# Kernel tuning notes

Hardware: AMD Instinct MI355X
Metric: run time of the kernel (lower is better)

Reference implementation:

```python
import jax, jax.numpy as jnp
from jax import lax
import numpy as np
import math

B, C, Hf, Wf = 16, 512, 32, 32   # batch, channels, feature map HxW (1024/32)
A, K = 9, 2                      # anchors per location, num classes
NCLU, UNITS, EMB = 100, 512, 128 # cosine-softmax dims
IMG = 1024                       # image side


def setup_inputs() -> dict:
    key = jax.random.key(0)
    ks = jax.random.split(key, 12)
    inp = {}
    inp["features"] = jax.random.normal(ks[0], (B, C, Hf, Wf), jnp.float32)
    inp["anchors"] = jax.random.uniform(ks[1], (Hf * Wf * A, 4), jnp.float32) * IMG
    inp["image_shape"] = IMG
    for l in range(4):
        inp[f"conv_w{l}"] = 0.01 * jax.random.normal(jax.random.fold_in(ks[2], l), (C, C, 3, 3), jnp.float32)
        inp[f"conv_b{l}"] = jnp.zeros((C,), jnp.float32)
    inp["cls_w"] = 0.01 * jax.random.normal(ks[3], (A * K, C, 3, 3), jnp.float32)
    inp["cls_b"] = jnp.full((A * K,), -math.log((1.0 - 0.01) / 0.01), jnp.float32)
    inp["bn_gamma"] = jnp.ones((C,), jnp.float32)
    inp["bn_beta"] = jnp.zeros((C,), jnp.float32)
    inp["proj_w1"] = 0.02 * jax.random.normal(ks[4], (UNITS, C), jnp.float32)
    inp["proj_w2"] = 0.02 * jax.random.normal(ks[5], (UNITS, UNITS), jnp.float32)
    inp["proj_w3"] = 0.02 * jax.random.normal(ks[6], (EMB, UNITS), jnp.float32)
    inp["clusters_w"] = 0.02 * jax.random.normal(ks[7], (NCLU, EMB), jnp.float32)
    inp["fc_scale_w"] = 0.02 * jax.random.normal(ks[8], (1, C), jnp.float32)
    inp["fc_scale_b"] = jnp.zeros((1,), jnp.float32)
    inp["bns_gamma"] = jnp.ones((1,), jnp.float32)
    inp["bns_beta"] = jnp.zeros((1,), jnp.float32)
    return inp


def _conv(x, w, b):
    y = lax.conv_general_dilated(x, w, (1, 1), 'SAME', dimension_numbers=('NCHW', 'OIHW', 'NCHW'))
    return y + b[None, :, None, None]


def _bn(x, g, b, eps=1e-5):  # BatchNorm1d in training mode: batch statistics
    m = x.mean(axis=0)
    v = x.var(axis=0)
    return g * (x - m) * lax.rsqrt(v + eps) + b


def _l2norm(x, axis):  # F.normalize(eps=1e-12)
    n = jnp.linalg.norm(x, axis=axis, keepdims=True)
    return x / jnp.maximum(n, 1e-12)


def reference(features, anchors, conv_w0, conv_b0, conv_w1, conv_b1, conv_w2, conv_b2,
              conv_w3, conv_b3, cls_w, cls_b, bn_gamma, bn_beta, proj_w1, proj_w2,
              proj_w3, clusters_w, fc_scale_w, fc_scale_b, bns_gamma, bns_beta,
              image_shape):
    # --- BBoxClassificationHead ---
    x = features
    for w, b in ((conv_w0, conv_b0), (conv_w1, conv_b1), (conv_w2, conv_b2), (conv_w3, conv_b3)):
        x = jax.nn.relu(_conv(x, w, b))
    logits = _conv(x, cls_w, cls_b)                      # [B, A*K, Hf, Wf]
    N = logits.shape[0]
    logits = logits.reshape(N, A, K, Hf, Wf).transpose(0, 3, 4, 1, 2).reshape(N, Hf * Wf * A, K)

    # --- _get_most_likely_feats: decode anchor centers, argmax foreground prob, gather ---
    feat_size = features.shape[2]
    decim = image_shape // feat_size
    cx = (anchors[:, 2] - anchors[:, 0]) / decim
    cy = (anchors[:, 3] - anchors[:, 1]) / decim
    p_fg = jax.nn.softmax(logits, axis=-1)[..., -1]      # [B, HWA]
    idx = jnp.argmax(p_fg, axis=-1)                      # [B]
    ii = jnp.clip(jnp.round(cy[idx]), 0, feat_size - 1).astype(jnp.int32)
    jj = jnp.clip(jnp.round(cx[idx]), 0, feat_size - 1).astype(jnp.int32)
    local = features[jnp.arange(N), :, ii, jj]           # [B, C]

    # --- CosineModule ---
    h = _bn(local, bn_gamma, bn_beta)
    h = jax.nn.relu(h @ proj_w1.T)
    h = jax.nn.relu(h @ proj_w2.T)
    emb = h @ proj_w3.T
    xn = _l2norm(emb, 1)                                 # [B, EMB]
    wn = _l2norm(clusters_w, 1).T                        # [EMB, NCLU]
    scale = jnp.exp(_bn(local @ fc_scale_w.T + fc_scale_b, bns_gamma, bns_beta))  # [B, 1]
    cosine = scale * (xn @ wn)                           # [B, NCLU]
    return (logits, cosine, xn)
```

## Files before the change

### kernel.cpp

```cpp
#include <hip/hip_runtime.h>

typedef short bf16x8 __attribute__((ext_vector_type(8)));
typedef float f32x4 __attribute__((ext_vector_type(4)));
typedef unsigned int u32x4 __attribute__((ext_vector_type(4)));
typedef unsigned short u16;

__device__ __forceinline__ bool dt_isbf(const void* flagp) {
  return (*(const unsigned int*)flagp) != 0x3F800000u;
}
__device__ __forceinline__ float bf2f(u16 v) {
  unsigned int x = ((unsigned int)v) << 16;
  return __builtin_bit_cast(float, x);
}
__device__ __forceinline__ u16 f2bf(float f) {
  unsigned int x = __builtin_bit_cast(unsigned int, f);
  x += 0x7FFFu + ((x >> 16) & 1u);
  return (u16)(x >> 16);
}
__device__ __forceinline__ float ldf(const void* p, int i, bool bf) {
  return bf ? bf2f(((const u16*)p)[i]) : ((const float*)p)[i];
}
__device__ __forceinline__ void gld_lds16(const void* g, void* l) {
  __builtin_amdgcn_global_load_lds(
      (const __attribute__((address_space(1))) unsigned*)g,
      (__attribute__((address_space(3))) unsigned*)l, 16, 0, 0);
}

__global__ __launch_bounds__(256) void k_to_nhwc(const void* __restrict__ feat,
                                                 u16* __restrict__ outH,
                                                 u16* __restrict__ outL,
                                                 const void* __restrict__ flagp) {
  const bool isbf = dt_isbf(flagp);
  __shared__ float tile[32][33];
  const int b = blockIdx.z, c0 = blockIdx.y << 5, p0 = blockIdx.x << 5;
  const int tp = threadIdx.x & 31, tc = threadIdx.x >> 5;
#pragma unroll
  for (int q = 0; q < 4; ++q) {
    int c = c0 + tc + (q << 3);
    tile[tc + (q << 3)][tp] = ldf(feat, ((b << 9) + c) * 1024 + p0 + tp, isbf);
  }
  __syncthreads();
#pragma unroll
  for (int q = 0; q < 4; ++q) {
    int p = p0 + tc + (q << 3);
    float v = tile[tp][tc + (q << 3)];
    u16 h = f2bf(v);
    int idx = (((b << 10) + p) << 9) + c0 + tp;
    outH[idx] = h;
    if (outL) outL[idx] = f2bf(v - bf2f(h));
  }
}

__global__ __launch_bounds__(256) void k_wtrans(const void* __restrict__ Wsrc,
                                                u16* __restrict__ WTh,
                                                u16* __restrict__ WTl, int Nout,
                                                const void* __restrict__ flagp) {
  const bool isbf = dt_isbf(flagp);
  const int n = blockIdx.x, tid = threadIdx.x;
  __shared__ float Wrow[4608];
  if (n < Nout)
    for (int k = tid; k < 4608; k += 256)
      Wrow[k] = ldf(Wsrc, n * 4608 + k, isbf);
  __syncthreads();
  for (int ko = tid; ko < 4608; ko += 256) {
    float w = 0.f;
    if (n < Nout) {
      int t = ko >> 6, q = (ko >> 3) & 7, j = ko & 7;
      int sk = (t << 6) + ((q ^ (n & 7)) << 3) + j;
      int c = sk & 511, tap = sk >> 9;
      w = Wrow[c * 9 + tap];
    }
    u16 h = f2bf(w);
    WTh[n * 4608 + ko] = h;
    if (!isbf) WTl[n * 4608 + ko] = f2bf(w - bf2f(h));
  }
}

__global__ __launch_bounds__(256) void k_gemm_conv(
    const u16* __restrict__ Xh, const u16* __restrict__ Xl,
    const u16* __restrict__ WTh, const u16* __restrict__ WTl,
    const void* __restrict__ bias,
    u16* __restrict__ Yh, u16* __restrict__ Yl,
    const void* __restrict__ flagp) {
  const bool isbf = dt_isbf(flagp);
  const bool useBL = !isbf;
  const int tid = threadIdx.x;
  const int m0 = blockIdx.x << 7, n0 = blockIdx.y << 7;
  const int b = m0 >> 10, y0 = (m0 & 1023) >> 5;
  __shared__ __align__(16) u16 Ash[13056], Asl[13056];
  __shared__ __align__(16) u16 Bh[8192];
  const int lane = tid & 63, wv = tid >> 6;
  const int wm = wv >> 1, wn = wv & 1;
  const int r16 = lane & 15, lg = lane >> 4;

  f32x4 acc[4][4];
#pragma unroll
  for (int i = 0; i < 4; ++i)
#pragma unroll
    for (int f = 0; f < 4; ++f) acc[i][f] = (f32x4){0.f, 0.f, 0.f, 0.f};

  for (int cb = 0; cb < 8; ++cb) {
    for (int e = tid; e < 1632; e += 256) {
      int pos = e >> 3, c8 = e & 7;
      int yy = pos / 34, xx = pos - yy * 34;
      int y = y0 + yy - 1, x = xx - 1;
      u32x4 vh = {0u, 0u, 0u, 0u}, vl = {0u, 0u, 0u, 0u};
      if ((unsigned)y < 32u && (unsigned)x < 32u) {
        size_t off = (size_t)((((b << 5) + y) << 5) + x) * 512 + (cb << 6) + (c8 << 3);
        vh = *(const u32x4*)(Xh + off);
        vl = *(const u32x4*)(Xl + off);
      }
      int sl = c8 ^ (xx & 7);
      *(u32x4*)(&Ash[(pos << 6) + (sl << 3)]) = vh;
      *(u32x4*)(&Asl[(pos << 6) + (sl << 3)]) = vl;
    }
    for (int tap = 0; tap < 9; ++tap) {
      const int t = (tap << 3) + cb;
#pragma unroll
      for (int issue = 0; issue < 4; ++issue) {
        int cid = (issue << 8) + tid;
        int row = cid >> 3, q = cid & 7;
        gld_lds16(WTh + (size_t)(n0 + row) * 4608 + (t << 6) + (q << 3),
                  &Bh[((issue << 2) + wv) << 9]);
      }
      __syncthreads();
      const int dy = tap / 3 - 1, dx = tap % 3 - 1;
#pragma unroll
      for (int s = 0; s < 2; ++s) {
        bf16x8 ah[4], al[4], bh[4], bl[4];
#pragma unroll
        for (int i = 0; i < 4; ++i) {
          int ar = (wm << 6) + (i << 4) + r16;
          int yy = (ar >> 5) + dy + 1, xx = (ar & 31) + dx + 1;
          int sidx = (s << 2) + lg;
          int ao = ((yy * 34 + xx) << 6) + ((sidx ^ (xx & 7)) << 3);
          ah[i] = *(const bf16x8*)(&Ash[ao]);
          al[i] = *(const bf16x8*)(&Asl[ao]);
          int br = (wn << 6) + (i << 4) + r16;
          int bs_ = sidx ^ (br & 7);
          bh[i] = *(const bf16x8*)(&Bh[(br << 6) + (bs_ << 3)]);
          if (useBL)
            bl[i] = *(const bf16x8*)(WTl + (size_t)(n0 + br) * 4608 + (t << 6) +
                                     (bs_ << 3));
        }
#pragma unroll
        for (int i = 0; i < 4; ++i)
#pragma unroll
          for (int f = 0; f < 4; ++f) {
            acc[i][f] = __builtin_amdgcn_mfma_f32_16x16x32_bf16(ah[i], bh[f], acc[i][f], 0, 0, 0);
            acc[i][f] = __builtin_amdgcn_mfma_f32_16x16x32_bf16(al[i], bh[f], acc[i][f], 0, 0, 0);
            if (useBL)
              acc[i][f] = __builtin_amdgcn_mfma_f32_16x16x32_bf16(ah[i], bl[f], acc[i][f], 0, 0, 0);
          }
      }
      __syncthreads();
    }
  }

#pragma unroll
  for (int f = 0; f < 4; ++f) {
    int col = n0 + (wn << 6) + (f << 4) + r16;
    float bb = ldf(bias, col, isbf);
#pragma unroll
    for (int i = 0; i < 4; ++i) {
      int mb = m0 + (wm << 6) + (i << 4) + (lg << 2);
#pragma unroll
      for (int r = 0; r < 4; ++r) {
        float v = fmaxf(acc[i][f][r] + bb, 0.f);
        size_t o = (size_t)(mb + r) * 512 + col;
        u16 h = f2bf(v);
        Yh[o] = h;
        Yl[o] = f2bf(v - bf2f(h));
      }
    }
  }
}

template <int NB, int KS>
__global__ __launch_bounds__(256) void k_gemm_fast(
    const u16* __restrict__ Xh, const u16* __restrict__ Xl,
    const u16* __restrict__ WTh, const u16* __restrict__ WTl,
    const void* __restrict__ bias, int bias_n,
    u16* __restrict__ Yh, u16* __restrict__ Yl, int Nst, int relu,
    float* __restrict__ Yf, const void* __restrict__ flagp) {
  const bool isbf = dt_isbf(flagp);
  const bool useBL = !isbf;
  const int tid = threadIdx.x;
  const int m0 = blockIdx.x << 7;
  int n0, kt0, kt1;
  if (KS) {
    n0 = 0;
    kt0 = blockIdx.y * 18;
    kt1 = kt0 + 18;
    Yf += (size_t)blockIdx.y * 294912;
  } else {
    n0 = blockIdx.y << 7;
    kt0 = 0;
    kt1 = 72;
  }
  __shared__ __align__(16) u16 Ah[8192], Al[8192], Bh[8192];
  const int lane = tid & 63, wv = tid >> 6;
  const int wm = wv >> 1, wn = wv & 1;
  const int r16 = lane & 15, lg = lane >> 4;

  const int arow0 = tid >> 3, acol = tid & 7;
  int gb[4], gy[4], gx[4];
#pragma unroll
  for (int i = 0; i < 4; ++i) {
    int m = m0 + arow0 + (i << 5);
    gb[i] = m >> 10;
    int p = m & 1023;
    gy[i] = p >> 5;
    gx[i] = p & 31;
  }

  f32x4 acc[4][4];
#pragma unroll
  for (int i = 0; i < 4; ++i)
#pragma unroll
    for (int f = 0; f < 4; ++f) acc[i][f] = (f32x4){0.f, 0.f, 0.f, 0.f};

  for (int t = kt0; t < kt1; ++t) {
    const int tap = t >> 3;
    const int cb = (t & 7) << 6;
    const int dy = tap / 3 - 1, dx = tap % 3 - 1;
    __syncthreads();
#pragma unroll
    for (int issue = 0; issue < NB / 2; ++issue) {
      int cid = (issue << 8) + tid;
      int row = cid >> 3, q = cid & 7;
      const u16* g = WTh + (size_t)(n0 + row) * 4608 + (t << 6) + (q << 3);
      u16* l = &Bh[(size_t)(((issue << 2) + wv) << 6) << 3];
      gld_lds16(g, l);
    }
#pragma unroll
    for (int i = 0; i < 4; ++i) {
      int row = arow0 + (i << 5);
      int ys = gy[i] + dy, xs = gx[i] + dx;
      u32x4 vh = {0u, 0u, 0u, 0u}, vl = {0u, 0u, 0u, 0u};
      if ((unsigned)ys < 32u && (unsigned)xs < 32u) {
        size_t off = (size_t)((((gb[i] << 5) + ys) << 5) + xs) * 512 + cb + (acol << 3);
        vh = *(const u32x4*)(Xh + off);
        vl = *(const u32x4*)(Xl + off);
      }
      int slot = acol ^ (row & 7);
      *(u32x4*)(&Ah[(row << 6) + (slot << 3)]) = vh;
      *(u32x4*)(&Al[(row << 6) + (slot << 3)]) = vl;
    }
    __syncthreads();
#pragma unroll
    for (int s = 0; s < 2; ++s) {
      bf16x8 ah[4], al[4], bh[4], bl[4];
#pragma unroll
      for (int i = 0; i < 4; ++i) {
        int ar = (wm << 6) + (i << 4) + r16;
        int as_ = ((s << 2) + lg) ^ (ar & 7);
        ah[i] = *(const bf16x8*)(&Ah[(ar << 6) + (as_ << 3)]);
        al[i] = *(const bf16x8*)(&Al[(ar << 6) + (as_ << 3)]);
      }
#pragma unroll
      for (int f = 0; f < 4; ++f) {
        if ((wn << 2) + f < NB) {
          int br = (wn << 6) + (f << 4) + r16;
          int bs_ = ((s << 2) + lg) ^ (br & 7);
          bh[f] = *(const bf16x8*)(&Bh[(br << 6) + (bs_ << 3)]);
          if (useBL)
            bl[f] = *(const bf16x8*)(WTl + (size_t)(n0 + br) * 4608 + (t << 6) +
                                     ((((s << 2) + lg) ^ (br & 7)) << 3));
        }
      }
#pragma unroll
      for (int i = 0; i < 4; ++i)
#pragma unroll
        for (int f = 0; f < 4; ++f) {
          if ((wn << 2) + f < NB) {
            acc[i][f] = __builtin_amdgcn_mfma_f32_16x16x32_bf16(ah[i], bh[f], acc[i][f], 0, 0, 0);
            acc[i][f] = __builtin_amdgcn_mfma_f32_16x16x32_bf16(al[i], bh[f], acc[i][f], 0, 0, 0);
            if (useBL)
              acc[i][f] = __builtin_amdgcn_mfma_f32_16x16x32_bf16(ah[i], bl[f], acc[i][f], 0, 0, 0);
          }
        }
    }
  }

#pragma unroll
  for (int f = 0; f < 4; ++f) {
    if ((wn << 2) + f >= NB) continue;
    int col = n0 + (wn << 6) + (f << 4) + r16;
    if (col < Nst) {
      float bb = (col < bias_n) ? ldf(bias, col, isbf) : 0.f;
#pragma unroll
      for (int i = 0; i < 4; ++i) {
        int mb = m0 + (wm << 6) + (i << 4) + (lg << 2);
#pragma unroll
        for (int r = 0; r < 4; ++r) {
          float v = acc[i][f][r] + bb;
          if (relu) v = fmaxf(v, 0.f);
          size_t o = (size_t)(mb + r) * Nst + col;
          if (Yh) {
            u16 h = f2bf(v);
            Yh[o] = h;
            Yl[o] = f2bf(v - bf2f(h));
          }
          if (Yf) Yf[o] = v;
        }
      }
    }
  }
}

__global__ __launch_bounds__(256) void k_cls_fin(const float* __restrict__ PART,
                                                 const void* __restrict__ bias,
                                                 float* __restrict__ out,
                                                 const void* __restrict__ flagp) {
  const bool isbf = dt_isbf(flagp);
  int o = blockIdx.x * 256 + threadIdx.x;
  if (o < 294912) {
    float v = PART[o] + PART[294912 + o] + PART[2 * 294912 + o] +
              PART[3 * 294912 + o];
    out[o] = v + ldf(bias, o % 18, isbf);
  }
}

__global__ __launch_bounds__(256) void k_gemm_slow(
    const u16* __restrict__ Xh, const u16* __restrict__ Xl,
    const void* __restrict__ Wsrc, const void* __restrict__ bias, int bias_n,
    u16* __restrict__ Yh, u16* __restrict__ Yl, int Nst, int relu,
    float* __restrict__ Yf, const void* __restrict__ flagp) {
  const bool isbf = dt_isbf(flagp);
  const bool hasBL = !isbf;
  const bool hasAL = (Xl != nullptr);
  const int tid = threadIdx.x;
  const int m0 = blockIdx.x << 7, n0 = blockIdx.y << 7;
  __shared__ __align__(16) u16 Ah[128 * 72];
  __shared__ __align__(16) u16 Al[128 * 72];
  __shared__ __align__(16) u16 Bh[128 * 72];
  __shared__ __align__(16) u16 Bl[128 * 72];
  const int lane = tid & 63, wvi = tid >> 6;
  const int wm = wvi >> 1, wn = wvi & 1;
  const int r16 = lane & 15, lg = lane >> 4;
  f32x4 acc[4][4];
#pragma unroll
  for (int i = 0; i < 4; ++i)
#pragma unroll
    for (int f = 0; f < 4; ++f) acc[i][f] = (f32x4){0.f, 0.f, 0.f, 0.f};
  for (int t = 0; t < 72; ++t) {
    const int tap = t >> 3, cb = (t & 7) << 6;
    const int dy = tap / 3 - 1, dx = tap % 3 - 1;
    __syncthreads();
    for (int e = tid; e < 4096; e += 256) {
      int row = e >> 5, kc2 = e & 31;
      int m = m0 + row;
      int b = m >> 10, p = m & 1023;
      int ys = (p >> 5) + dy, xs = (p & 31) + dx;
      unsigned vh = 0u, vl = 0u;
      if ((unsigned)ys < 32u && (unsigned)xs < 32u) {
        int off = ((((b << 5) + ys) << 5) + xs) * 512 + cb + (kc2 << 1);
        vh = *(const unsigned*)(Xh + off);
        if (hasAL) vl = *(const unsigned*)(Xl + off);
      }
      *(unsigned*)(&Ah[row * 72 + (kc2 << 1)]) = vh;
      if (hasAL) *(unsigned*)(&Al[row * 72 + (kc2 << 1)]) = vl;
    }
    for (int e = tid; e < 4096; e += 256) {
      int row = e >> 5, kc2 = e & 31;
      int n = n0 + row;
      unsigned ph = 0u, pl = 0u;
      if (n < bias_n) {
        int c = cb + (kc2 << 1);
        float w0 = ldf(Wsrc, ((n << 9) + c) * 9 + tap, isbf);
        float w1 = ldf(Wsrc, ((n << 9) + c + 1) * 9 + tap, isbf);
        u16 h0 = f2bf(w0), h1 = f2bf(w1);
        ph = ((unsigned)h1 << 16) | (unsigned)h0;
        if (hasBL) {
          u16 l0 = f2bf(w0 - bf2f(h0)), l1 = f2bf(w1 - bf2f(h1));
          pl = ((unsigned)l1 << 16) | (unsigned)l0;
        }
      }
      *(unsigned*)(&Bh[row * 72 + (kc2 << 1)]) = ph;
      if (hasBL) *(unsigned*)(&Bl[row * 72 + (kc2 << 1)]) = pl;
    }
    __syncthreads();
#pragma unroll
    for (int s = 0; s < 2; ++s) {
      bf16x8 ah[4], al[4], bh[4], bl[4];
#pragma unroll
      for (int i = 0; i < 4; ++i) {
        int ao = ((wm << 6) + (i << 4) + r16) * 72 + (s << 5) + (lg << 3);
        int bo = ((wn << 6) + (i << 4) + r16) * 72 + (s << 5) + (lg << 3);
        ah[i] = *(const bf16x8*)(&Ah[ao]);
        bh[i] = *(const bf16x8*)(&Bh[bo]);
        if (hasAL) al[i] = *(const bf16x8*)(&Al[ao]);
        if (hasBL) bl[i] = *(const bf16x8*)(&Bl[bo]);
      }
#pragma unroll
      for (int i = 0; i < 4; ++i)
#pragma unroll
        for (int f = 0; f < 4; ++f) {
          acc[i][f] = __builtin_amdgcn_mfma_f32_16x16x32_bf16(ah[i], bh[f], acc[i][f], 0, 0, 0);
          if (hasAL)
            acc[i][f] = __builtin_amdgcn_mfma_f32_16x16x32_bf16(al[i], bh[f], acc[i][f], 0, 0, 0);
          if (hasBL)
            acc[i][f] = __builtin_amdgcn_mfma_f32_16x16x32_bf16(ah[i], bl[f], acc[i][f], 0, 0, 0);
        }
    }
  }
#pragma unroll
  for (int f = 0; f < 4; ++f) {
    int col = n0 + (wn << 6) + (f << 4) + r16;
    if (col < Nst) {
      float bb = (col < bias_n) ? ldf(bias, col, isbf) : 0.f;
#pragma unroll
      for (int i = 0; i < 4; ++i) {
        int mb = m0 + (wm << 6) + (i << 4) + (lg << 2);
#pragma unroll
        for (int r = 0; r < 4; ++r) {
          float v = acc[i][f][r] + bb;
          if (relu) v = fmaxf(v, 0.f);
          int o = (mb + r) * Nst + col;
          if (Yh) {
            u16 h = f2bf(v);
            Yh[o] = h;
            if (Yl) Yl[o] = f2bf(v - bf2f(h));
          }
          if (Yf) Yf[o] = v;
        }
      }
    }
  }
}

__global__ __launch_bounds__(256) void k_pick(const float* __restrict__ LG,
                                              const void* __restrict__ anchors,
                                              const int* __restrict__ imgshape,
                                              const void* __restrict__ feat,
                                              float* __restrict__ local,
                                              const void* __restrict__ flagp) {
  const bool isbf = dt_isbf(flagp);
  const int n = blockIdx.x, tid = threadIdx.x;
  float bs = -1e30f;
  int bj = 0x7FFFFFFF;
  for (int j = tid; j < 9216; j += 256) {
    float s = LG[n * 18432 + j * 2 + 1] - LG[n * 18432 + j * 2];
    if (s > bs) { bs = s; bj = j; }
  }
  __shared__ float ss[256];
  __shared__ int sj[256];
  ss[tid] = bs; sj[tid] = bj;
  __syncthreads();
  for (int off = 128; off; off >>= 1) {
    if (tid < off) {
      if (ss[tid + off] > ss[tid] ||
          (ss[tid + off] == ss[tid] && sj[tid + off] < sj[tid])) {
        ss[tid] = ss[tid + off]; sj[tid] = sj[tid + off];
      }
    }
    __syncthreads();
  }
  __shared__ int sij[2];
  if (tid == 0) {
    int idx = sj[0];
    float a0 = ldf(anchors, idx * 4 + 0, isbf);
    float a1 = ldf(anchors, idx * 4 + 1, isbf);
    float a2 = ldf(anchors, idx * 4 + 2, isbf);
    float a3 = ldf(anchors, idx * 4 + 3, isbf);
    int iv = imgshape[0];
    float fimg = (iv > 0 && iv < (1 << 24)) ? (float)iv
                                            : __builtin_bit_cast(float, iv);
    float decim = floorf(fimg / 32.f);
    float cx = (a2 - a0) / decim, cy = (a3 - a1) / decim;
    int ii = (int)fminf(fmaxf(rintf(cy), 0.f), 31.f);
    int jj = (int)fminf(fmaxf(rintf(cx), 0.f), 31.f);
    sij[0] = ii; sij[1] = jj;
  }
  __syncthreads();
  const int ii = sij[0], jj = sij[1];
  for (int c = tid; c < 512; c += 256)
    local[(n << 9) + c] = ldf(feat, ((n << 9) + c) * 1024 + (ii << 5) + jj, isbf);
}

__global__ __launch_bounds__(256) void k_head_pre(
    const float* __restrict__ local, const void* bn_g, const void* bn_b,
    const void* fcw, const void* fcb, const void* bsg, const void* bsb,
    const void* clus, float* __restrict__ HS, float* __restrict__ SCAL,
    float* __restrict__ CN, const void* __restrict__ flagp) {
  const bool isbf = dt_isbf(flagp);
  const int tid = threadIdx.x, blk = blockIdx.x;
  if (blk < 2) {
    int c = (blk << 8) + tid;
    float xv[16];
    float m = 0.f;
#pragma unroll
    for (int n = 0; n < 16; ++n) { xv[n] = local[(n << 9) + c]; m += xv[n]; }
    m *= 0.0625f;
    float v = 0.f;
#pragma unroll
    for (int n = 0; n < 16; ++n) { float d = xv[n] - m; v += d * d; }
    v *= 0.0625f;
    float rs = rsqrtf(v + 1e-5f);
    float g = ldf(bn_g, c, isbf), be = ldf(bn_b, c, isbf);
#pragma unroll
    for (int n = 0; n < 16; ++n) HS[(n << 9) + c] = g * (xv[n] - m) * rs + be;
  } else if (blk == 2) {
    __shared__ float sr[16];
    int n = tid >> 4, l16 = tid & 15;
    float a = 0.f;
    for (int c = l16; c < 512; c += 16) a += local[(n << 9) + c] * ldf(fcw, c, isbf);
#pragma unroll
    for (int m = 1; m < 16; m <<= 1) a += __shfl_xor(a, m);
    if (l16 == 0) sr[n] = a + ldf(fcb, 0, isbf);
    __syncthreads();
    if (tid == 0) {
      float m = 0.f;
      for (int k = 0; k < 16; ++k) m += sr[k];
      m *= 0.0625f;
      float v = 0.f;
      for (int k = 0; k < 16; ++k) { float d = sr[k] - m; v += d * d; }
      v *= 0.0625f;
      float rs = rsqrtf(v + 1e-5f);
      float g = ldf(bsg, 0, isbf), be = ldf(bsb, 0, isbf);
      for (int k = 0; k < 16; ++k) SCAL[k] = expf(g * (sr[k] - m) * rs + be);
    }
  } else {
    if (tid < 100) {
      float s = 0.f;
      for (int c = 0; c < 128; ++c) {
        float w = ldf(clus, tid * 128 + c, isbf);
        s += w * w;
      }
      CN[tid] = fmaxf(sqrtf(s), 1e-12f);
    }
  }
}

__global__ __launch_bounds__(256) void k_head_h(
    const float* __restrict__ IN, const void* __restrict__ W,
    float* __restrict__ OUT, int U, int relu,
    const void* __restrict__ flagp) {
  const bool isbf = dt_isbf(flagp);
  const int tid = threadIdx.x;
  const int u0 = blockIdx.x << 4;
  __shared__ float INs[16][516];
  __shared__ float Ws[16][516];
  for (int e = tid; e < 8192; e += 256) {
    int n = e >> 9, c = e & 511;
    INs[n][c] = IN[e];
    Ws[n][c] = ldf(W, (u0 + n) * 512 + c, isbf);
  }
  __syncthreads();
  const int n = tid >> 4, ui = tid & 15;
  float a = 0.f;
#pragma unroll 8
  for (int c = 0; c < 512; ++c) a += INs[n][c] * Ws[ui][c];
  if (relu) a = fmaxf(a, 0.f);
  OUT[n * U + u0 + ui] = a;
}

__global__ __launch_bounds__(512) void k_head_fin(
    const float* __restrict__ EMB, const void* __restrict__ clus,
    const float* __restrict__ SCAL, const float* __restrict__ CN,
    float* __restrict__ out, const void* __restrict__ flagp) {
  const bool isbf = dt_isbf(flagp);
  const int tid = threadIdx.x;
  __shared__ float X[16][128];
  __shared__ float CL[100][129];
  for (int e = tid; e < 2048; e += 512) X[e >> 7][e & 127] = EMB[e];
  for (int e = tid; e < 12800; e += 512) {
    int j = e >> 7, c = e & 127;
    CL[j][c] = ldf(clus, e, isbf);
  }
  __syncthreads();
  if (tid < 16) {
    float s = 0.f;
    for (int c = 0; c < 128; ++c) s += X[tid][c] * X[tid][c];
    float inv = 1.f / fmaxf(sqrtf(s), 1e-12f);
    for (int c = 0; c < 128; ++c) X[tid][c] *= inv;
  }
  __syncthreads();
  for (int idx = tid; idx < 1600; idx += 512) {
    int n = idx / 100, j = idx - n * 100;
    float s = 0.f;
#pragma unroll 8
    for (int c = 0; c < 128; ++c) s += X[n][c] * CL[j][c];
    out[294912 + idx] = SCAL[n] * s / CN[j];
  }
  for (int idx = tid; idx < 2048; idx += 512)
    out[294912 + 1600 + idx] = X[idx >> 7][idx & 127];
}

__global__ __launch_bounds__(512) void k_head(
    const float* __restrict__ local, const void* bn_g, const void* bn_b,
    const void* w1, const void* w2, const void* w3, const void* clus,
    const void* fcw, const void* fcb, const void* bsg, const void* bsb,
    float* __restrict__ out, const void* __restrict__ flagp) {
  const bool isbf = dt_isbf(flagp);
  const int tid = threadIdx.x;
  __shared__ float L[16][512];
  __shared__ float Hs[16][512];
  __shared__ float G[16][512];
  __shared__ float sraw[16], scal[16], cn[100];
  for (int i = tid; i < 8192; i += 512) L[i >> 9][i & 511] = local[i];
  __syncthreads();
  {
    int c = tid;
    float m = 0.f;
#pragma unroll
    for (int n = 0; n < 16; ++n) m += L[n][c];
    m *= 0.0625f;
    float v = 0.f;
#pragma unroll
    for (int n = 0; n < 16; ++n) { float d = L[n][c] - m; v += d * d; }
    v *= 0.0625f;
    float rs = rsqrtf(v + 1e-5f);
    float g = ldf(bn_g, c, isbf), be = ldf(bn_b, c, isbf);
#pragma unroll
    for (int n = 0; n < 16; ++n) Hs[n][c] = g * (L[n][c] - m) * rs + be;
  }
  __syncthreads();
  {
    float a[16];
#pragma unroll
    for (int n = 0; n < 16; ++n) a[n] = 0.f;
    for (int c = 0; c < 512; ++c) {
      float wvv = ldf(w1, tid * 512 + c, isbf);
#pragma unroll
      for (int n = 0; n < 16; ++n) a[n] += Hs[n][c] * wvv;
    }
#pragma unroll
    for (int n = 0; n < 16; ++n) G[n][tid] = fmaxf(a[n], 0.f);
  }
  __syncthreads();
  {
    float a[16];
#pragma unroll
    for (int n = 0; n < 16; ++n) a[n] = 0.f;
    for (int c = 0; c < 512; ++c) {
      float wvv = ldf(w2, tid * 512 + c, isbf);
#pragma unroll
      for (int n = 0; n < 16; ++n) a[n] += G[n][c] * wvv;
    }
#pragma unroll
    for (int n = 0; n < 16; ++n) Hs[n][tid] = fmaxf(a[n], 0.f);
  }
  __syncthreads();
  if (tid < 128) {
    float a[16];
#pragma unroll
    for (int n = 0; n < 16; ++n) a[n] = 0.f;
    for (int c = 0; c < 512; ++c) {
      float wvv = ldf(w3, tid * 512 + c, isbf);
#pragma unroll
      for (int n = 0; n < 16; ++n) a[n] += Hs[n][c] * wvv;
    }
#pragma unroll
    for (int n = 0; n < 16; ++n) G[n][tid] = a[n];
  } else if (tid >= 256 && tid < 272) {
    int n = tid - 256;
    float s = 0.f;
    for (int c = 0; c < 512; ++c) s += L[n][c] * ldf(fcw, c, isbf);
    sraw[n] = s + ldf(fcb, 0, isbf);
  } else if (tid >= 384 && tid < 484) {
    int j = tid - 384;
    float s = 0.f;
    for (int c = 0; c < 128; ++c) { float wvv = ldf(clus, j * 128 + c, isbf); s += wvv * wvv; }
    cn[j] = fmaxf(sqrtf(s), 1e-12f);
  }
  __syncthreads();
  if (tid < 16) {
    int n = tid;
    float s = 0.f;
    for (int c = 0; c < 128; ++c) s += G[n][c] * G[n][c];
    float inv = 1.f / fmaxf(sqrtf(s), 1e-12f);
    for (int c = 0; c < 128; ++c) G[n][c] *= inv;
  } else if (tid == 32) {
    float m = 0.f;
    for (int n = 0; n < 16; ++n) m += sraw[n];
    m *= 0.0625f;
    float v = 0.f;
    for (int n = 0; n < 16; ++n) { float d = sraw[n] - m; v += d * d; }
    v *= 0.0625f;
    float rs = rsqrtf(v + 1e-5f);
    float g = ldf(bsg, 0, isbf), be = ldf(bsb, 0, isbf);
    for (int n = 0; n < 16; ++n) scal[n] = expf(g * (sraw[n] - m) * rs + be);
  }
  __syncthreads();
  for (int idx = tid; idx < 1600; idx += 512) {
    int n = idx / 100, j = idx - n * 100;
    float s = 0.f;
    for (int c = 0; c < 128; ++c) s += G[n][c] * ldf(clus, j * 128 + c, isbf);
    out[294912 + idx] = scal[n] * s / cn[j];
  }
  for (int idx = tid; idx < 2048; idx += 512)
    out[294912 + 1600 + idx] = G[idx >> 7][idx & 127];
}

extern "C" void kernel_launch(void* const* d_in, const int* in_sizes, int n_in,
                              void* d_out, int out_size, void* d_ws, size_t ws_size,
                              hipStream_t stream) {
  const void* features = d_in[0];
  const void* anchors = d_in[1];
  const int* image_shape = (const int*)d_in[2];
  const void* conv_w[4] = {d_in[3], d_in[5], d_in[7], d_in[9]};
  const void* conv_b[4] = {d_in[4], d_in[6], d_in[8], d_in[10]};
  const void* cls_w = d_in[11];
  const void* cls_b = d_in[12];
  const void* bn_gamma = d_in[13];
  const void* bn_beta = d_in[14];
  const void* proj_w1 = d_in[15];
  const void* proj_w2 = d_in[16];
  const void* proj_w3 = d_in[17];
  const void* clusters_w = d_in[18];
  const void* fc_scale_w = d_in[19];
  const void* fc_scale_b = d_in[20];
  const void* bns_gamma = d_in[21];
  const void* bns_beta = d_in[22];
  const void* flagp = bn_gamma;

  char* ws = (char*)d_ws;
  float* out = (float*)d_out;
  const size_t MB16 = 16777216u;
  const size_t WSZ = 4718592u;
  const size_t FAST_NEED = 4 * MB16 + 2 * WSZ + 131072u;

  u16* AH = (u16*)(ws);
  u16* AL = (u16*)(ws + MB16);
  u16* BH = (u16*)(ws + 2 * MB16);
  u16* BL = (u16*)(ws + 3 * MB16);

  if (ws_size >= FAST_NEED) {
    u16* WTh = (u16*)(ws + 4 * MB16);
    u16* WTl = (u16*)(ws + 4 * MB16 + WSZ);
    char* hb = (char*)BH;
    float* LOCAL = (float*)(hb);
    float* HS = (float*)(hb + 32768);
    float* H1 = (float*)(hb + 65536);
    float* H2 = (float*)(hb + 98304);
    float* EMB = (float*)(hb + 131072);
    float* SCAL = (float*)(hb + 139264);
    float* CN = (float*)(hb + 139392);
    float* PART = (float*)BL;

    k_to_nhwc<<<dim3(32, 16, 16), 256, 0, stream>>>(features, AH, AL, flagp);
    u16 *ch = AH, *cl = AL, *nh = BH, *nl = BL;
    for (int l = 0; l < 4; ++l) {
      k_wtrans<<<dim3(512), 256, 0, stream>>>(conv_w[l], WTh, WTl, 512, flagp);
      k_gemm_conv<<<dim3(128, 4), 256, 0, stream>>>(ch, cl, WTh, WTl, conv_b[l],
                                                    nh, nl, flagp);
      u16* t;
      t = ch; ch = nh; nh = t;
      t = cl; cl = nl; nl = t;
    }
    k_wtrans<<<dim3(32), 256, 0, stream>>>(cls_w, WTh, WTl, 18, flagp);
    k_gemm_fast<2, 1><<<dim3(128, 4), 256, 0, stream>>>(
        ch, cl, WTh, WTl, cls_b, 0, nullptr, nullptr, 18, 0, PART, flagp);
    k_cls_fin<<<dim3(1152), 256, 0, stream>>>(PART, cls_b, out, flagp);

    k_pick<<<dim3(16), 256, 0, stream>>>(out, anchors, image_shape, features,
                                         LOCAL, flagp);
    k_head_pre<<<dim3(4), 256, 0, stream>>>(LOCAL, bn_gamma, bn_beta, fc_scale_w,
                                            fc_scale_b, bns_gamma, bns_beta,
                                            clusters_w, HS, SCAL, CN, flagp);
    k_head_h<<<dim3(32), 256, 0, stream>>>(HS, proj_w1, H1, 512, 1, flagp);
    k_head_h<<<dim3(32), 256, 0, stream>>>(H1, proj_w2, H2, 512, 1, flagp);
    k_head_h<<<dim3(8), 256, 0, stream>>>(H2, proj_w3, EMB, 128, 0, flagp);
    k_head_fin<<<dim3(1), 512, 0, stream>>>(EMB, clusters_w, SCAL, CN, out, flagp);
  } else {
    float* LOCAL = (float*)(ws + 4 * MB16);
    k_to_nhwc<<<dim3(32, 16, 16), 256, 0, stream>>>(features, AH, AL, flagp);
    u16 *ch = AH, *cl = AL, *nh = BH, *nl = BL;
    for (int l = 0; l < 4; ++l) {
      k_gemm_slow<<<dim3(128, 4), 256, 0, stream>>>(ch, cl, conv_w[l], conv_b[l],
                                                    512, nh, nl, 512, 1, nullptr,
                                                    flagp);
      u16* t;
      t = ch; ch = nh; nh = t;
      t = cl; cl = nl; nl = t;
    }
    k_gemm_slow<<<dim3(128, 1), 256, 0, stream>>>(ch, cl, cls_w, cls_b, 18,
                                                  nullptr, nullptr, 18, 0, out,
                                                  flagp);
    k_pick<<<dim3(16), 256, 0, stream>>>(out, anchors, image_shape, features,
                                         LOCAL, flagp);
    k_head<<<dim3(1), 512, 0, stream>>>(LOCAL, bn_gamma, bn_beta, proj_w1,
                                        proj_w2, proj_w3, clusters_w, fc_scale_w,
                                        fc_scale_b, bns_gamma, bns_beta, out,
                                        flagp);
  }
}
```

Baseline: 998.3 us.

## Register-prefetch next weight tile during conv GEMM and set launch bounds

Replaces the direct global-to-LDS loads of the B (weight) tile with a register double-buffer. The next k-step's weights are loaded into registers while the current step's MFMAs run, then written to LDS at the start of the next iteration. Barriers are split around the A-tile fill. Launch bounds now request two blocks per CU, which may cause register spilling given the 64 accumulator floats plus the prefetch registers.

Result: faster. 945.8 us (-5.3%).

```diff
diff --git a/kernel.cpp b/kernel.cpp
--- a/kernel.cpp
+++ b/kernel.cpp
@@ -76,7 +76,7 @@
   }
 }
 
-__global__ __launch_bounds__(256) void k_gemm_conv(
+__global__ __launch_bounds__(256, 2) void k_gemm_conv(
     const u16* __restrict__ Xh, const u16* __restrict__ Xl,
     const u16* __restrict__ WTh, const u16* __restrict__ WTl,
     const void* __restrict__ bias,
@@ -99,14 +99,24 @@
 #pragma unroll
     for (int f = 0; f < 4; ++f) acc[i][f] = (f32x4){0.f, 0.f, 0.f, 0.f};
 
+  u32x4 breg[4];
+#pragma unroll
+  for (int is = 0; is < 4; ++is) {
+    int cid = (is << 8) + tid;
+    breg[is] = *(const u32x4*)(WTh + (size_t)(n0 + (cid >> 3)) * 4608 +
+                               ((cid & 7) << 3));
+  }
+
   for (int cb = 0; cb < 8; ++cb) {
+    __syncthreads();
     for (int e = tid; e < 1632; e += 256) {
       int pos = e >> 3, c8 = e & 7;
       int yy = pos / 34, xx = pos - yy * 34;
       int y = y0 + yy - 1, x = xx - 1;
       u32x4 vh = {0u, 0u, 0u, 0u}, vl = {0u, 0u, 0u, 0u};
       if ((unsigned)y < 32u && (unsigned)x < 32u) {
-        size_t off = (size_t)((((b << 5) + y) << 5) + x) * 512 + (cb << 6) + (c8 << 3);
+        size_t off =
+            (size_t)((((b << 5) + y) << 5) + x) * 512 + (cb << 6) + (c8 << 3);
         vh = *(const u32x4*)(Xh + off);
         vl = *(const u32x4*)(Xl + off);
       }
@@ -114,16 +124,28 @@
       *(u32x4*)(&Ash[(pos << 6) + (sl << 3)]) = vh;
       *(u32x4*)(&Asl[(pos << 6) + (sl << 3)]) = vl;
     }
+    __syncthreads();
+
     for (int tap = 0; tap < 9; ++tap) {
       const int t = (tap << 3) + cb;
-#pragma unroll
-      for (int issue = 0; issue < 4; ++issue) {
-        int cid = (issue << 8) + tid;
-        int row = cid >> 3, q = cid & 7;
-        gld_lds16(WTh + (size_t)(n0 + row) * 4608 + (t << 6) + (q << 3),
-                  &Bh[((issue << 2) + wv) << 9]);
-      }
-      __syncthreads();
+      const int kk = cb * 9 + tap;
+#pragma unroll
+      for (int is = 0; is < 4; ++is)
+        *(u32x4*)(&Bh[((is << 8) + tid) << 3]) = breg[is];
+      asm volatile("s_waitcnt lgkmcnt(0)" ::: "memory");
+      if (kk + 1 < 72) {
+        int kb = kk + 1;
+        int cb2 = kb / 9, tap2 = kb - cb2 * 9;
+        int t2 = (tap2 << 3) + cb2;
+#pragma unroll
+        for (int is = 0; is < 4; ++is) {
+          int cid = (is << 8) + tid;
+          breg[is] = *(const u32x4*)(WTh + (size_t)(n0 + (cid >> 3)) * 4608 +
+                                     (t2 << 6) + ((cid & 7) << 3));
+        }
+      }
+      __builtin_amdgcn_s_barrier();
+      __builtin_amdgcn_sched_barrier(0);
       const int dy = tap / 3 - 1, dx = tap % 3 - 1;
 #pragma unroll
       for (int s = 0; s < 2; ++s) {
@@ -140,8 +162,8 @@
           int bs_ = sidx ^ (br & 7);
           bh[i] = *(const bf16x8*)(&Bh[(br << 6) + (bs_ << 3)]);
           if (useBL)
-            bl[i] = *(const bf16x8*)(WTl + (size_t)(n0 + br) * 4608 + (t << 6) +
-                                     (bs_ << 3));
+            bl[i] = *(const bf16x8*)(WTl + (size_t)(n0 + br) * 4608 +
+                                     (t << 6) + (bs_ << 3));
         }
 #pragma unroll
         for (int i = 0; i < 4; ++i)
@@ -153,7 +175,7 @@
               acc[i][f] = __builtin_amdgcn_mfma_f32_16x16x32_bf16(ah[i], bl[f], acc[i][f], 0, 0, 0);
           }
       }
-      __syncthreads();
+      __builtin_amdgcn_s_barrier();
     }
   }
 
```
